# Optimization experiments

Measured on AMD Instinct MI355X. Metric: run time of the kernel, lower is better.

## Reference

```python
import jax, jax.numpy as jnp
import numpy as np

N_NODES = 16384
N_EDGES = 131072
EDGE_DIM = 16
IN_CH = 32
OUT_CH = 32
HID_EDGE = 64
MLP_HID = 64  # int(32 * 2.0)
OUT_FINAL = 10
N_GRAPHS = 64
BN_EPS = 1e-5


def setup_inputs() -> dict:
    key = jax.random.key(0)
    ks = jax.random.split(key, 20)
    s = lambda *sh: 1.0 / np.sqrt(sh[0])
    inp = {
        'x': jax.random.normal(ks[0], (N_NODES, IN_CH), jnp.float32),
        'edge_attr': jax.random.normal(ks[1], (N_EDGES, EDGE_DIM), jnp.float32),
        'edge_index': jax.random.randint(ks[2], (2, N_EDGES), 0, N_NODES, jnp.int64),
        'batch': jnp.sort(jax.random.randint(ks[3], (N_NODES,), 0, N_GRAPHS, jnp.int64)),
    }
    # layer 0: edge MLP (EDGE_DIM->HID_EDGE->IN_CH*OUT_CH), root, bias, BN affine
    inp['w1_0'] = jax.random.normal(ks[4], (EDGE_DIM, HID_EDGE), jnp.float32) * s(EDGE_DIM)
    inp['b1_0'] = jnp.zeros((HID_EDGE,), jnp.float32)
    inp['w2_0'] = jax.random.normal(ks[5], (HID_EDGE, IN_CH * OUT_CH), jnp.float32) * s(HID_EDGE)
    inp['b2_0'] = jnp.zeros((IN_CH * OUT_CH,), jnp.float32)
    inp['root_0'] = jax.random.normal(ks[6], (IN_CH, OUT_CH), jnp.float32) * s(IN_CH)
    inp['bias_0'] = jnp.zeros((OUT_CH,), jnp.float32)
    inp['gamma_0'] = jnp.ones((OUT_CH,), jnp.float32)
    inp['beta_0'] = jnp.zeros((OUT_CH,), jnp.float32)
    # layer 1: edge MLP (EDGE_DIM->HID_EDGE->OUT_CH*OUT_CH)
    inp['w1_1'] = jax.random.normal(ks[7], (EDGE_DIM, HID_EDGE), jnp.float32) * s(EDGE_DIM)
    inp['b1_1'] = jnp.zeros((HID_EDGE,), jnp.float32)
    inp['w2_1'] = jax.random.normal(ks[8], (HID_EDGE, OUT_CH * OUT_CH), jnp.float32) * s(HID_EDGE)
    inp['b2_1'] = jnp.zeros((OUT_CH * OUT_CH,), jnp.float32)
    inp['root_1'] = jax.random.normal(ks[9], (OUT_CH, OUT_CH), jnp.float32) * s(OUT_CH)
    inp['bias_1'] = jnp.zeros((OUT_CH,), jnp.float32)
    inp['gamma_1'] = jnp.ones((OUT_CH,), jnp.float32)
    inp['beta_1'] = jnp.zeros((OUT_CH,), jnp.float32)
    # final MLP (dropout is identity in eval / deterministic reference)
    inp['mlp_w1'] = jax.random.normal(ks[10], (OUT_CH, MLP_HID), jnp.float32) * s(OUT_CH)
    inp['mlp_b1'] = jnp.zeros((MLP_HID,), jnp.float32)
    inp['mlp_w2'] = jax.random.normal(ks[11], (MLP_HID, OUT_FINAL), jnp.float32) * s(MLP_HID)
    inp['mlp_b2'] = jnp.zeros((OUT_FINAL,), jnp.float32)
    return inp


def _nnconv(x, src, dst, edge_attr, w1, b1, w2, b2, root, bias, out_ch):
    # per-edge weight matrices from the edge MLP: [E, in, out]
    h = jax.nn.relu(edge_attr @ w1 + b1)
    W = (h @ w2 + b2).reshape(-1, x.shape[1], out_ch)
    msg = jnp.einsum('ei,eio->eo', x[src], W)  # gather + per-edge matmul
    agg = jax.ops.segment_sum(msg, dst, num_segments=N_NODES)
    cnt = jax.ops.segment_sum(jnp.ones((dst.shape[0], 1), x.dtype), dst, num_segments=N_NODES)
    agg = agg / jnp.maximum(cnt, 1.0)  # scatter-mean (zero-degree nodes -> 0)
    return agg + x @ root + bias


def _bn(x, gamma, beta):
    m = jnp.mean(x, axis=0)
    v = jnp.var(x, axis=0)
    return (x - m) * jax.lax.rsqrt(v + BN_EPS) * gamma + beta


def reference(x, edge_attr, edge_index, batch,
              w1_0, b1_0, w2_0, b2_0, root_0, bias_0, gamma_0, beta_0,
              w1_1, b1_1, w2_1, b2_1, root_1, bias_1, gamma_1, beta_1,
              mlp_w1, mlp_b1, mlp_w2, mlp_b2):
    src, dst = edge_index[0], edge_index[1]
    h = _nnconv(x, src, dst, edge_attr, w1_0, b1_0, w2_0, b2_0, root_0, bias_0, OUT_CH)
    h = jax.nn.relu(_bn(h, gamma_0, beta_0))
    h = _nnconv(h, src, dst, edge_attr, w1_1, b1_1, w2_1, b2_1, root_1, bias_1, OUT_CH)
    h = jax.nn.relu(_bn(h, gamma_1, beta_1))
    # global mean pool over graphs
    pooled = jax.ops.segment_sum(h, batch, num_segments=N_GRAPHS)
    gcnt = jax.ops.segment_sum(jnp.ones((h.shape[0], 1), h.dtype), batch, num_segments=N_GRAPHS)
    pooled = pooled / jnp.maximum(gcnt, 1.0)
    logits = jax.nn.relu(pooled @ mlp_w1 + mlp_b1) @ mlp_w2 + mlp_b2
    return logits
```

## Files before the change

### kernel.cpp

```cpp
#include <hip/hip_runtime.h>
#include <hip/hip_bf16.h>

#define NN 16384
#define NE 131072
#define NG 64
#define EPB 128

typedef unsigned short u16;
typedef unsigned int u32;
typedef __attribute__((ext_vector_type(8))) short short8;
typedef __attribute__((ext_vector_type(4))) float f32x4;
typedef __attribute__((ext_vector_type(8))) _Float16 f16x8;
typedef __attribute__((ext_vector_type(2))) _Float16 f16x2;
typedef __attribute__((address_space(1))) const unsigned int gu32;
typedef __attribute__((address_space(3))) unsigned int lu32;

__device__ __forceinline__ float bf2f(u16 u) {
    u32 x = ((u32)u) << 16;
    return __builtin_bit_cast(float, x);
}
__device__ __forceinline__ u16 f2bf(float f) {
    u32 u = __builtin_bit_cast(u32, f);
    u = u + 0x7fffu + ((u >> 16) & 1u);
    return (u16)(u >> 16);
}
__device__ __forceinline__ u16 f2h(float f) {
    _Float16 h = (_Float16)f;
    return __builtin_bit_cast(u16, h);
}
__device__ __forceinline__ f16x2 pkrtz(float a, float b) {
    auto v = __builtin_amdgcn_cvt_pkrtz(a, b);
    static_assert(sizeof(v) == 4, "pkrtz size");
    return __builtin_bit_cast(f16x2, v);
}
#if __has_builtin(__builtin_amdgcn_cvt_pk_bf16_f32)
__device__ __forceinline__ u32 pk2bf_fast(float a, float b) {
    auto v = __builtin_amdgcn_cvt_pk_bf16_f32(a, b);
    static_assert(sizeof(v) == 4, "cvt_pk_bf16 size");
    return __builtin_bit_cast(u32, v);
}
#else
__device__ __forceinline__ u32 pk2bf_fast(float a, float b) {
    u32 ua = __builtin_bit_cast(u32, a) + 0x8000u;
    u32 ub = __builtin_bit_cast(u32, b) + 0x8000u;
    return __builtin_amdgcn_perm(ub, ua, 0x07060302u);
}
#endif
__device__ __forceinline__ float loadF(const void* p, int i, bool bf) {
    return bf ? bf2f(((const u16*)p)[i]) : ((const float*)p)[i];
}
__device__ __forceinline__ int loadI(const void* p, int i, bool i64) {
    return i64 ? (int)((const long long*)p)[i] : ((const int*)p)[i];
}
__device__ __forceinline__ bool det_bf(const void* g0) {
    return ((const u16*)g0)[0] == 0x3F80u;
}
__device__ __forceinline__ bool det_i64(const void* eidx) {
    const u32* u = (const u32*)eidx;
    return (u[1] | u[3] | u[5] | u[7]) == 0u;
}

__global__ __launch_bounds__(256) void k_prep(const void* w2a, const void* b2a,
                                              const void* w2b, const void* b2b,
                                              const void* w1a, const void* w1b,
                                              u16* bp0, u16* bp1, u16* w1p0, u16* w1p1,
                                              const void* eidx, float* cnt, u32* eord,
                                              const void* g0) {
    const bool bf = det_bf(g0);
    int id = blockIdx.x * 256 + threadIdx.x;
    if (id < 2 * 66560) {
        int l = id / 66560, v = id % 66560;
        int j = v & 7, lane = (v >> 3) & 63, nt = (v >> 9) & 1, t = v >> 10;
        int kk = (lane >> 4) * 8 + j;
        int n = (lane & 15) + 16 * nt;
        const void* w2 = l ? w2b : w2a;
        const void* b2 = l ? b2b : b2a;
        float val = (t < 64) ? loadF(w2, t * 1024 + kk * 32 + n, bf)
                             : loadF(b2, kk * 32 + n, bf);
        (l ? bp1 : bp0)[v] = f2h(val);
    } else if (id < 2 * 66560 + 2 * 2048) {
        int v = id - 2 * 66560;
        int l = v >> 11; v &= 2047;
        int j = v & 7, lane = (v >> 3) & 63, nt = v >> 9;
        int k = (lane >> 4) * 8 + j;
        int n = nt * 16 + (lane & 15);
        const void* w1 = l ? w1b : w1a;
        float val = (k < 16) ? loadF(w1, k * 64 + n, bf) : 0.f;
        (l ? w1p1 : w1p0)[v] = f2bf(val);
    } else {
        const bool i64 = det_i64(eidx);
        int e = id - (2 * 66560 + 2 * 2048);
        int d = loadI(eidx, NE + e, i64);
        int slot = (int)atomicAdd(&cnt[d], 1.0f);
        if (slot < 64) eord[d * 64 + slot] = (u32)e;
    }
}

__device__ __forceinline__ void stage_chunk(const u16* Bpack, u16* lds, int cc, int w, int lane) {
    const char* src = (const char*)Bpack + (size_t)cc * 8192 + (size_t)(w * 1024 + lane * 16);
    char* dst = (char*)lds + w * 1024;
    __builtin_amdgcn_global_load_lds((gu32*)src, (lu32*)dst, 16, 0, 0);
    __builtin_amdgcn_global_load_lds((gu32*)(src + 4096), (lu32*)(dst + 4096), 16, 0, 0);
}

#define HSTR 72
__global__ __launch_bounds__(256, 4) void k_edge(const void* ea, const u16* w1p, const void* b1,
                                                 const void* xv, int layer1,
                                                 const float* sSp, const float* sQp,
                                                 const void* gammap, const void* betap,
                                                 const void* eidx, const u16* Bpack,
                                                 float* msg, const void* g0) {
    const bool bf = det_bf(g0);
    const bool i64 = det_i64(eidx);
    __shared__ __align__(16) u16 hl[EPB * HSTR];
    __shared__ __align__(16) u16 Bls[2][4096];
    __shared__ __align__(16) float bnS[32], bnB[32];
    const int tid = threadIdx.x;
    const int e0 = blockIdx.x * EPB;
    const int lane = tid & 63;
    const int w = tid >> 6;
    const int q = lane >> 4;
    const int m = lane & 15;
    const int wbl = w * 32;
    const int wb = e0 + wbl;

    stage_chunk(Bpack, Bls[0], 0, w, lane);
    stage_chunk(Bpack, Bls[1], 1, w, lane);

    if (layer1 && tid < 32) {
        float s = 0.f, qq = 0.f;
#pragma unroll
        for (int p = 0; p < 16; p++) { s += sSp[p * 32 + tid]; qq += sQp[p * 32 + tid]; }
        float mn = s * (1.0f / 16384.0f);
        float var = qq * (1.0f / 16384.0f) - mn * mn;
        float inv = rsqrtf(var + 1e-5f);
        float g = loadF(gammap, tid, bf), b = loadF(betap, tid, bf);
        bnS[tid] = inv * g;
        bnB[tid] = b - mn * inv * g;
    }

    {
        short8 Ah[2];
#pragma unroll
        for (int e2 = 0; e2 < 2; e2++) {
            int eg = wb + e2 * 16 + m;
            uint4 av = make_uint4(0u, 0u, 0u, 0u);
            if (bf) {
                uint4 t = *(const uint4*)((const char*)ea + (size_t)eg * 32 + (q & 1) * 16);
                if (q < 2) av = t;
            } else {
                const float4* p = (const float4*)((const char*)ea + (size_t)eg * 64 + (q & 1) * 32);
                float4 a = p[0], b = p[1];
                if (q < 2) av = make_uint4(pk2bf_fast(a.x, a.y), pk2bf_fast(a.z, a.w),
                                           pk2bf_fast(b.x, b.y), pk2bf_fast(b.z, b.w));
            }
            Ah[e2] = __builtin_bit_cast(short8, av);
        }
#pragma unroll
        for (int nt = 0; nt < 4; nt++) {
            uint4 bw = *(const uint4*)&w1p[(nt * 64 + lane) * 8];
            short8 Bf = __builtin_bit_cast(short8, bw);
            float bb = loadF(b1, nt * 16 + m, bf);
#pragma unroll
            for (int e2 = 0; e2 < 2; e2++) {
                f32x4 c = __builtin_amdgcn_mfma_f32_16x16x32_bf16(
                    Ah[e2], Bf, f32x4{0.f, 0.f, 0.f, 0.f}, 0, 0, 0);
                int rbase = (wbl + e2 * 16 + q * 4) * HSTR + nt * 16 + m;
#pragma unroll
                for (int r = 0; r < 4; r++) {
                    _Float16 hv = (_Float16)fmaxf(c[r] + bb, 0.f);
                    hl[rbase + r * HSTR] = __builtin_bit_cast(u16, hv);
                }
            }
        }
    }

    float4 ga[2], gb[2];
#pragma unroll
    for (int mt = 0; mt < 2; mt++) {
        int s = loadI(eidx, wb + mt * 16 + m, i64);
        if (layer1 || !bf) {
            const float4* xp = (const float4*)xv + (size_t)s * 8 + q * 2;
            ga[mt] = xp[0]; gb[mt] = xp[1];
        } else {
            const uint4* xp = (const uint4*)((const char*)xv + (size_t)s * 64 + q * 16);
            uint4 a = *xp;
            ga[mt] = make_float4(bf2f((u16)(a.x & 0xffff)), bf2f((u16)(a.x >> 16)),
                                 bf2f((u16)(a.y & 0xffff)), bf2f((u16)(a.y >> 16)));
            gb[mt] = make_float4(bf2f((u16)(a.z & 0xffff)), bf2f((u16)(a.z >> 16)),
                                 bf2f((u16)(a.w & 0xffff)), bf2f((u16)(a.w >> 16)));
        }
    }

    __syncthreads();

    f16x2 xh[2][4];
    if (layer1) {
        float4 s0 = *(const float4*)&bnS[q * 8], s1 = *(const float4*)&bnS[q * 8 + 4];
        float4 h0 = *(const float4*)&bnB[q * 8], h1 = *(const float4*)&bnB[q * 8 + 4];
#pragma unroll
        for (int mt = 0; mt < 2; mt++) {
            xh[mt][0] = pkrtz(fmaxf(ga[mt].x * s0.x + h0.x, 0.f), fmaxf(ga[mt].y * s0.y + h0.y, 0.f));
            xh[mt][1] = pkrtz(fmaxf(ga[mt].z * s0.z + h0.z, 0.f), fmaxf(ga[mt].w * s0.w + h0.w, 0.f));
            xh[mt][2] = pkrtz(fmaxf(gb[mt].x * s1.x + h1.x, 0.f), fmaxf(gb[mt].y * s1.y + h1.y, 0.f));
            xh[mt][3] = pkrtz(fmaxf(gb[mt].z * s1.z + h1.z, 0.f), fmaxf(gb[mt].w * s1.w + h1.w, 0.f));
        }
    } else {
#pragma unroll
        for (int mt = 0; mt < 2; mt++) {
            xh[mt][0] = pkrtz(ga[mt].x, ga[mt].y);
            xh[mt][1] = pkrtz(ga[mt].z, ga[mt].w);
            xh[mt][2] = pkrtz(gb[mt].x, gb[mt].y);
            xh[mt][3] = pkrtz(gb[mt].z, gb[mt].w);
        }
    }

    f32x4 acc[2][2];
#pragma unroll
    for (int mt = 0; mt < 2; mt++) {
        acc[mt][0] = f32x4{0.f, 0.f, 0.f, 0.f};
        acc[mt][1] = f32x4{0.f, 0.f, 0.f, 0.f};
    }
    int rowb[2];
#pragma unroll
    for (int mt = 0; mt < 2; mt++) rowb[mt] = (wbl + mt * 16 + m) * HSTR;

    for (int cc = 0; cc < 16; cc++) {
        uint2 hw[2];
        hw[0] = *(const uint2*)&hl[rowb[0] + cc * 4];
        hw[1] = *(const uint2*)&hl[rowb[1] + cc * 4];
        const u16* Bb = &Bls[cc & 1][lane * 8];
#pragma unroll
        for (int tt = 0; tt < 4; tt++) {
            uint4 bu0 = *(const uint4*)(Bb + (tt * 2 + 0) * 512);
            uint4 bu1 = *(const uint4*)(Bb + (tt * 2 + 1) * 512);
            f16x8 B0 = __builtin_bit_cast(f16x8, bu0);
            f16x8 B1 = __builtin_bit_cast(f16x8, bu1);
            const u32 sel = (tt & 1) ? 0x03020302u : 0x01000100u;
#pragma unroll
            for (int mt = 0; mt < 2; mt++) {
                u32 wd = (tt & 2) ? hw[mt].y : hw[mt].x;
                u32 hh = __builtin_amdgcn_perm(wd, wd, sel);
                f16x2 h2 = __builtin_bit_cast(f16x2, hh);
                f16x2 p0 = h2 * xh[mt][0];
                f16x2 p1 = h2 * xh[mt][1];
                f16x2 p2 = h2 * xh[mt][2];
                f16x2 p3 = h2 * xh[mt][3];
                uint4 au = make_uint4(__builtin_bit_cast(u32, p0), __builtin_bit_cast(u32, p1),
                                      __builtin_bit_cast(u32, p2), __builtin_bit_cast(u32, p3));
                f16x8 A = __builtin_bit_cast(f16x8, au);
                acc[mt][0] = __builtin_amdgcn_mfma_f32_16x16x32_f16(A, B0, acc[mt][0], 0, 0, 0);
                acc[mt][1] = __builtin_amdgcn_mfma_f32_16x16x32_f16(A, B1, acc[mt][1], 0, 0, 0);
            }
        }
        __syncthreads();
        if (cc < 15) stage_chunk(Bpack, Bls[cc & 1], cc + 2, w, lane);
    }
    {
        const u16* Bb = &Bls[0][lane * 8];
        uint4 bu0 = *(const uint4*)(Bb + 0);
        uint4 bu1 = *(const uint4*)(Bb + 512);
        f16x8 B0 = __builtin_bit_cast(f16x8, bu0);
        f16x8 B1 = __builtin_bit_cast(f16x8, bu1);
#pragma unroll
        for (int mt = 0; mt < 2; mt++) {
            uint4 au = make_uint4(__builtin_bit_cast(u32, xh[mt][0]), __builtin_bit_cast(u32, xh[mt][1]),
                                  __builtin_bit_cast(u32, xh[mt][2]), __builtin_bit_cast(u32, xh[mt][3]));
            f16x8 A = __builtin_bit_cast(f16x8, au);
            acc[mt][0] = __builtin_amdgcn_mfma_f32_16x16x32_f16(A, B0, acc[mt][0], 0, 0, 0);
            acc[mt][1] = __builtin_amdgcn_mfma_f32_16x16x32_f16(A, B1, acc[mt][1], 0, 0, 0);
        }
    }

#pragma unroll
    for (int mt = 0; mt < 2; mt++) {
        float* mp = msg + (size_t)(wb + mt * 16 + q * 4) * 32 + m;
#pragma unroll
        for (int r = 0; r < 4; r++) {
            mp[r * 32] = acc[mt][0][r];
            mp[r * 32 + 16] = acc[mt][1][r];
        }
    }
}

__global__ __launch_bounds__(256) void k_node(const float* msg, const u32* eord, const float* cnt,
                                              const void* xv, int layer1,
                                              const float* sSp, const float* sQp,
                                              const void* gammap, const void* betap,
                                              const void* root, const void* bias,
                                              float* hpre, float* sS, float* sQ,
                                              const void* g0) {
    const bool bf = det_bf(g0);
    const int tid = threadIdx.x;
    const int v = blockIdx.x * 8 + (tid >> 5);
    const int o = tid & 31;
    __shared__ float bnS[32], bnB[32];
    if (layer1) {
        if (tid < 32) {
            float s = 0.f, qq = 0.f;
#pragma unroll
            for (int p = 0; p < 16; p++) { s += sSp[p * 32 + tid]; qq += sQp[p * 32 + tid]; }
            float mn = s * (1.0f / 16384.0f);
            float var = qq * (1.0f / 16384.0f) - mn * mn;
            float inv = rsqrtf(var + 1e-5f);
            float g = loadF(gammap, tid, bf), b = loadF(betap, tid, bf);
            bnS[tid] = inv * g;
            bnB[tid] = b - mn * inv * g;
        }
        __syncthreads();
    }
    float xrow[32];
    if (layer1) {
        const float4* x4 = (const float4*)((const float*)xv + (size_t)v * 32);
        float4 xa[8];
#pragma unroll
        for (int i = 0; i < 8; i++) xa[i] = x4[i];
        const float* xs = (const float*)xa;
#pragma unroll
        for (int i = 0; i < 32; i++) xrow[i] = fmaxf(xs[i] * bnS[i] + bnB[i], 0.f);
    } else if (!bf) {
        const float4* x4 = (const float4*)((const float*)xv + (size_t)v * 32);
        float4 xa[8];
#pragma unroll
        for (int i = 0; i < 8; i++) xa[i] = x4[i];
        const float* xs = (const float*)xa;
#pragma unroll
        for (int i = 0; i < 32; i++) xrow[i] = xs[i];
    } else {
        const u16* x = (const u16*)xv + (size_t)v * 32;
#pragma unroll
        for (int i = 0; i < 32; i++) xrow[i] = bf2f(x[i]);
    }
    float a;
    if (bf) {
        const u16* R = (const u16*)root;
        a = bf2f(((const u16*)bias)[o]);
#pragma unroll
        for (int i = 0; i < 32; i++) a += xrow[i] * bf2f(R[i * 32 + o]);
    } else {
        const float* R = (const float*)root;
        a = ((const float*)bias)[o];
#pragma unroll
        for (int i = 0; i < 32; i++) a += xrow[i] * R[i * 32 + o];
    }
    int deg = (int)cnt[v];
    if (deg > 64) deg = 64;
    const u32* ep = eord + (size_t)v * 64;
    float av0 = 0.f, av1 = 0.f;
    int j = 0;
    for (; j + 1 < deg; j += 2) {
        u32 ea0 = ep[j], ea1 = ep[j + 1];
        av0 += msg[(size_t)ea0 * 32 + o];
        av1 += msg[(size_t)ea1 * 32 + o];
    }
    if (j < deg) av0 += msg[(size_t)ep[j] * 32 + o];
    float pre = (av0 + av1) / fmaxf(cnt[v], 1.0f) + a;
    hpre[(size_t)v * 32 + o] = pre;

    __shared__ float lS[256], lQ[256];
    lS[tid] = pre;
    lQ[tid] = pre * pre;
    __syncthreads();
#pragma unroll
    for (int off = 128; off >= 32; off >>= 1) {
        if (tid < off) { lS[tid] += lS[tid + off]; lQ[tid] += lQ[tid + off]; }
        __syncthreads();
    }
    if (tid < 32) {
        int slot = (blockIdx.x & 15) * 32 + tid;
        atomicAdd(&sS[slot], lS[tid]);
        atomicAdd(&sQ[slot], lQ[tid]);
    }
}

__global__ __launch_bounds__(256) void k_tail(const float* hpre, const float* sS, const float* sQ,
                                              const void* gamma, const void* beta,
                                              const void* batch,
                                              const void* w1, const void* b1,
                                              const void* w2, const void* b2,
                                              void* out, const void* eidx, const void* g0) {
    const bool bf = det_bf(g0);
    const bool i64 = det_i64(eidx);
    const int g = blockIdx.x;
    const int tid = threadIdx.x;
    const int o = tid & 31;
    const int c = tid >> 5;
    __shared__ float lS[256];
    __shared__ float pool[32];

    float s = 0.f, qq = 0.f;
#pragma unroll
    for (int pp = 0; pp < 16; pp++) { s += sS[pp * 32 + o]; qq += sQ[pp * 32 + o]; }
    float mn = s * (1.0f / 16384.0f);
    float var = qq * (1.0f / 16384.0f) - mn * mn;
    float inv = rsqrtf(var + 1e-5f);
    float gg = loadF(gamma, o, bf), bb = loadF(beta, o, bf);

    int lo = 0, hi = NN;
    while (lo < hi) {
        int mid = (lo + hi) >> 1;
        if (loadI(batch, mid, i64) < g) lo = mid + 1; else hi = mid;
    }
    int lo2 = lo, hi2 = NN;
    while (lo2 < hi2) {
        int mid = (lo2 + hi2) >> 1;
        if (loadI(batch, mid, i64) < g + 1) lo2 = mid + 1; else hi2 = mid;
    }
    const int nbeg = lo, nend = lo2;

    float acc = 0.f;
    for (int v = nbeg + c; v < nend; v += 8)
        acc += fmaxf((hpre[(size_t)v * 32 + o] - mn) * inv * gg + bb, 0.f);
    lS[tid] = acc;
    __syncthreads();
#pragma unroll
    for (int off = 4; off >= 1; off >>= 1) {
        if (c < off) lS[tid] += lS[tid + off * 32];
        __syncthreads();
    }
    if (tid < 32) pool[o] = lS[o] / fmaxf((float)(nend - nbeg), 1.0f);
    __syncthreads();

    if (tid < 64) {
        float a = loadF(b1, tid, bf);
#pragma unroll
        for (int i = 0; i < 32; i++) a += pool[i] * loadF(w1, i * 64 + tid, bf);
        a = fmaxf(a, 0.f);
        float lg[10];
#pragma unroll
        for (int cc = 0; cc < 10; cc++) lg[cc] = a * loadF(w2, tid * 10 + cc, bf);
#pragma unroll
        for (int off = 32; off >= 1; off >>= 1) {
#pragma unroll
            for (int cc = 0; cc < 10; cc++) lg[cc] += __shfl_down(lg[cc], off, 64);
        }
        if (tid == 0) {
            if (bf) {
                u16* op = (u16*)out;
#pragma unroll
                for (int cc = 0; cc < 10; cc++) op[g * 10 + cc] = f2bf(lg[cc] + loadF(b2, cc, bf));
            } else {
                float* op = (float*)out;
#pragma unroll
                for (int cc = 0; cc < 10; cc++) op[g * 10 + cc] = lg[cc] + loadF(b2, cc, bf);
            }
        }
    }
}

extern "C" void kernel_launch(void* const* d_in, const int* in_sizes, int n_in,
                              void* d_out, int out_size, void* d_ws, size_t ws_size,
                              hipStream_t stream) {
    char* ws = (char*)d_ws;
    u16* bp0  = (u16*)(ws + 256);
    u16* bp1  = (u16*)(ws + 256 + 133120);
    u16* w1p0 = (u16*)(ws + 266496);
    u16* w1p1 = (u16*)(ws + 270592);
    char* zbase = ws + 274688;
    float* cnt    = (float*)(zbase);
    float* sS0    = (float*)(zbase + 65536);
    float* sQ0    = (float*)(zbase + 67584);
    float* sS1    = (float*)(zbase + 69632);
    float* sQ1    = (float*)(zbase + 71680);
    const size_t zsize = 73728;
    char* nz = zbase + 82176;
    u32*   eord  = (u32*)(nz);
    float* msg   = (float*)(nz + 4194304);
    float* hpre0 = (float*)(nz + 4194304 + 16777216);
    float* hpre1 = (float*)(nz + 4194304 + 16777216 + 2097152);

    const void* x     = d_in[0];
    const void* ea    = d_in[1];
    const void* eidx  = d_in[2];
    const void* batch = d_in[3];
    const void* g0    = d_in[10];

    (void)hipMemsetAsync(zbase, 0, zsize, stream);
    k_prep<<<1048, 256, 0, stream>>>(d_in[6], d_in[7], d_in[14], d_in[15],
                                     d_in[4], d_in[12],
                                     bp0, bp1, w1p0, w1p1, eidx, cnt, eord, g0);

    k_edge<<<NE / EPB, 256, 0, stream>>>(ea, w1p0, d_in[5], x, 0,
                                         nullptr, nullptr, nullptr, nullptr,
                                         eidx, bp0, msg, g0);
    k_node<<<NN / 8, 256, 0, stream>>>(msg, eord, cnt, x, 0,
                                       nullptr, nullptr, nullptr, nullptr,
                                       d_in[8], d_in[9], hpre0, sS0, sQ0, g0);

    k_edge<<<NE / EPB, 256, 0, stream>>>(ea, w1p1, d_in[13], hpre0, 1,
                                         sS0, sQ0, d_in[10], d_in[11],
                                         eidx, bp1, msg, g0);
    k_node<<<NN / 8, 256, 0, stream>>>(msg, eord, cnt, hpre0, 1,
                                       sS0, sQ0, d_in[10], d_in[11],
                                       d_in[16], d_in[17], hpre1, sS1, sQ1, g0);

    k_tail<<<NG, 256, 0, stream>>>(hpre1, sS1, sQ1, d_in[18], d_in[19], batch,
                                   d_in[20], d_in[21], d_in[22], d_in[23], d_out, eidx, g0);
}
```

Before: 211.8 us.

## Scatter edge messages into per-destination slots for contiguous node gathers

Edge messages are no longer written in edge order and gathered by index list. Each edge now writes its 32-float message directly into a padded per-destination bucket (node*64+slot). The node kernel can then sum messages contiguously without the indirection through eord. This removes the dependent index load and the random gather, but the edge kernel's stores become scattered and the message buffer grows to 128 MB with a sparse padded layout.

After: 204.9 us (median of 2 runs). -3.3%, faster.

```diff
diff --git a/kernel.cpp b/kernel.cpp
--- a/kernel.cpp
+++ b/kernel.cpp
@@ -64,7 +64,7 @@
                                               const void* w2b, const void* b2b,
                                               const void* w1a, const void* w1b,
                                               u16* bp0, u16* bp1, u16* w1p0, u16* w1p1,
-                                              const void* eidx, float* cnt, u32* eord,
+                                              const void* eidx, float* cnt, u32* eoff,
                                               const void* g0) {
     const bool bf = det_bf(g0);
     int id = blockIdx.x * 256 + threadIdx.x;
@@ -92,7 +92,7 @@
         int e = id - (2 * 66560 + 2 * 2048);
         int d = loadI(eidx, NE + e, i64);
         int slot = (int)atomicAdd(&cnt[d], 1.0f);
-        if (slot < 64) eord[d * 64 + slot] = (u32)e;
+        eoff[e] = (slot < 64) ? (u32)(d * 64 + slot) : 0xFFFFFFFFu;
     }
 }
 
@@ -109,7 +109,7 @@
                                                  const float* sSp, const float* sQp,
                                                  const void* gammap, const void* betap,
                                                  const void* eidx, const u16* Bpack,
-                                                 float* msg, const void* g0) {
+                                                 const u32* eoff, float* msgb, const void* g0) {
     const bool bf = det_bf(g0);
     const bool i64 = det_i64(eidx);
     __shared__ __align__(16) u16 hl[EPB * HSTR];
@@ -274,16 +274,20 @@
 
 #pragma unroll
     for (int mt = 0; mt < 2; mt++) {
-        float* mp = msg + (size_t)(wb + mt * 16 + q * 4) * 32 + m;
+        int eb = wb + mt * 16 + q * 4;
 #pragma unroll
         for (int r = 0; r < 4; r++) {
-            mp[r * 32] = acc[mt][0][r];
-            mp[r * 32 + 16] = acc[mt][1][r];
-        }
-    }
-}
-
-__global__ __launch_bounds__(256) void k_node(const float* msg, const u32* eord, const float* cnt,
+            u32 eo = eoff[eb + r];
+            if (eo != 0xFFFFFFFFu) {
+                float* mp = msgb + (size_t)eo * 32 + m;
+                mp[0] = acc[mt][0][r];
+                mp[16] = acc[mt][1][r];
+            }
+        }
+    }
+}
+
+__global__ __launch_bounds__(256) void k_node(const float* msgb, const float* cnt,
                                               const void* xv, int layer1,
                                               const float* sSp, const float* sQp,
                                               const void* gammap, const void* betap,
@@ -345,15 +349,14 @@
     }
     int deg = (int)cnt[v];
     if (deg > 64) deg = 64;
-    const u32* ep = eord + (size_t)v * 64;
+    const float* mb = msgb + (size_t)v * 2048 + o;
     float av0 = 0.f, av1 = 0.f;
     int j = 0;
     for (; j + 1 < deg; j += 2) {
-        u32 ea0 = ep[j], ea1 = ep[j + 1];
-        av0 += msg[(size_t)ea0 * 32 + o];
-        av1 += msg[(size_t)ea1 * 32 + o];
-    }
-    if (j < deg) av0 += msg[(size_t)ep[j] * 32 + o];
+        av0 += mb[(size_t)j * 32];
+        av1 += mb[(size_t)(j + 1) * 32];
+    }
+    if (j < deg) av0 += mb[(size_t)j * 32];
     float pre = (av0 + av1) / fmaxf(cnt[v], 1.0f) + a;
     hpre[(size_t)v * 32 + o] = pre;
 
@@ -463,11 +466,11 @@
     float* sS1    = (float*)(zbase + 69632);
     float* sQ1    = (float*)(zbase + 71680);
     const size_t zsize = 73728;
-    char* nz = zbase + 82176;
-    u32*   eord  = (u32*)(nz);
-    float* msg   = (float*)(nz + 4194304);
-    float* hpre0 = (float*)(nz + 4194304 + 16777216);
-    float* hpre1 = (float*)(nz + 4194304 + 16777216 + 2097152);
+    char* nz = zbase + 73728;
+    u32*   eoff  = (u32*)(nz);
+    float* msgb  = (float*)(nz + 524288);
+    float* hpre0 = (float*)(nz + 524288 + 134217728);
+    float* hpre1 = (float*)(nz + 524288 + 134217728 + 2097152);
 
     const void* x     = d_in[0];
     const void* ea    = d_in[1];
@@ -478,19 +481,19 @@
     (void)hipMemsetAsync(zbase, 0, zsize, stream);
     k_prep<<<1048, 256, 0, stream>>>(d_in[6], d_in[7], d_in[14], d_in[15],
                                      d_in[4], d_in[12],
-                                     bp0, bp1, w1p0, w1p1, eidx, cnt, eord, g0);
+                                     bp0, bp1, w1p0, w1p1, eidx, cnt, eoff, g0);
 
     k_edge<<<NE / EPB, 256, 0, stream>>>(ea, w1p0, d_in[5], x, 0,
                                          nullptr, nullptr, nullptr, nullptr,
-                                         eidx, bp0, msg, g0);
-    k_node<<<NN / 8, 256, 0, stream>>>(msg, eord, cnt, x, 0,
+                                         eidx, bp0, eoff, msgb, g0);
+    k_node<<<NN / 8, 256, 0, stream>>>(msgb, cnt, x, 0,
                                        nullptr, nullptr, nullptr, nullptr,
                                        d_in[8], d_in[9], hpre0, sS0, sQ0, g0);
 
     k_edge<<<NE / EPB, 256, 0, stream>>>(ea, w1p1, d_in[13], hpre0, 1,
                                          sS0, sQ0, d_in[10], d_in[11],
-                                         eidx, bp1, msg, g0);
-    k_node<<<NN / 8, 256, 0, stream>>>(msg, eord, cnt, hpre0, 1,
+                                         eidx, bp1, eoff, msgb, g0);
+    k_node<<<NN / 8, 256, 0, stream>>>(msgb, cnt, hpre0, 1,
                                        sS0, sQ0, d_in[10], d_in[11],
                                        d_in[16], d_in[17], hpre1, sS1, sQ1, g0);
 
```
